# Performance work log

Measured on AMD Instinct MI355X. Metric: run time of the kernel, lower is better.

The kernel has to match this reference:

```python
import jax, jax.numpy as jnp
import numpy as np

LN_EPS = 1e-5


def _conv2d(x, w, b, pad):
    # x: [B,C,H,W], w: [O,I,k,k] (torch OIHW layout)
    out = jax.lax.conv_general_dilated(
        x, w, (1, 1), [(pad, pad), (pad, pad)],
        dimension_numbers=('NCHW', 'OIHW', 'NCHW'))
    return out + b[None, :, None, None]


def _deform_conv2d(x, offset, w, b, k, pad):
    # torchvision.ops.deform_conv2d, offset_groups=1, stride=1, dilation=1.
    # offset layout: [B, 2*k*k, H, W] with (dy, dx) interleaved per kernel tap.
    B, C, H, W = x.shape
    off = offset.reshape(B, k * k, 2, H, W)
    dy, dx = off[:, :, 0], off[:, :, 1]                      # [B,kk,H,W]
    ky, kx = jnp.meshgrid(jnp.arange(k, dtype=x.dtype),
                          jnp.arange(k, dtype=x.dtype), indexing='ij')
    py = (jnp.arange(H, dtype=x.dtype)[None, None, :, None]
          - pad + ky.reshape(-1)[None, :, None, None] + dy)   # sample rows
    px = (jnp.arange(W, dtype=x.dtype)[None, None, None, :]
          - pad + kx.reshape(-1)[None, :, None, None] + dx)   # sample cols
    y0 = jnp.floor(py)
    x0 = jnp.floor(px)
    fy = py - y0
    fx = px - x0
    xf = x.reshape(B, C, H * W)
    gather = jax.vmap(lambda xb, ib: xb[:, ib])               # [C,HW],[K]->[C,K]

    def corner(yc, xc, wt):
        valid = (yc >= 0) & (yc < H) & (xc >= 0) & (xc < W)
        idx = (jnp.clip(yc, 0, H - 1) * W
               + jnp.clip(xc, 0, W - 1)).astype(jnp.int32).reshape(B, -1)
        g = gather(xf, idx).reshape(B, C, k * k, H, W)
        return g * (wt * valid.astype(x.dtype))[:, None]

    # bilinear sample with zero padding outside the image
    acc = (corner(y0, x0, (1 - fy) * (1 - fx))
           + corner(y0, x0 + 1, (1 - fy) * fx)
           + corner(y0 + 1, x0, fy * (1 - fx))
           + corner(y0 + 1, x0 + 1, fy * fx))                 # [B,C,kk,H,W]
    out = jnp.einsum('bckhw,ock->bohw', acc, w.reshape(w.shape[0], C, k * k))
    return out + b[None, :, None, None]


def _deform_branch(xs, off_w, off_b, conv_w, conv_b, k, pad):
    # DeformableConv2d.forward: offset conv, deform_conv2d with conv's own
    # weight/bias, then the plain conv applied AGAIN on the result.
    offset = _conv2d(xs, off_w, off_b, pad)
    d = _deform_conv2d(xs, offset, conv_w, conv_b, k, pad)
    return _conv2d(d, conv_w, conv_b, pad)


def reference(x, H, W, fc1_w, fc1_b, off3_w, off3_b, conv3_w, conv3_b,
              off5_w, off5_b, conv5_w, conv5_b, ln_g, ln_b, fc2_w, fc2_b):
    B, N, _ = x.shape
    h = x @ fc1_w.T + fc1_b                                  # [B,N,hid]
    C = h.shape[-1]
    C2 = C // 2
    x1 = jnp.transpose(h[..., :C2], (0, 2, 1)).reshape(B, C2, H, W)
    x2 = jnp.transpose(h[..., C2:], (0, 2, 1)).reshape(B, C2, H, W)
    x1 = _deform_branch(x1, off3_w, off3_b, conv3_w, conv3_b, 3, 1)
    x2 = _deform_branch(x2, off5_w, off5_b, conv5_w, conv5_b, 5, 2)
    y = jnp.concatenate([x1, x2], axis=1)                    # [B,C,H,W]
    y = jnp.transpose(y.reshape(B, C, N), (0, 2, 1))         # [B,N,C]
    mu = jnp.mean(y, axis=-1, keepdims=True)
    var = jnp.mean(jnp.square(y - mu), axis=-1, keepdims=True)
    y = (y - mu) * jax.lax.rsqrt(var + LN_EPS) * ln_g + ln_b
    y = jax.nn.gelu(y, approximate=False)                    # nn.GELU default
    return y @ fc2_w.T + fc2_b


def setup_inputs() -> dict:
    key = jax.random.key(0)
    ks = jax.random.split(key, 16)
    B, H, W, Cin, Chid = 4, 32, 32, 256, 1024
    C2 = Chid // 2
    N = H * W
    r = lambda k, s, sc: jax.random.normal(k, s, dtype=jnp.float32) * sc
    return {
        'x': r(ks[0], (B, N, Cin), 1.0),
        'H': H, 'W': W,
        'fc1_w': r(ks[1], (Chid, Cin), 0.02),
        'fc1_b': r(ks[2], (Chid,), 0.02),
        'off3_w': r(ks[3], (2 * 9, C2, 3, 3), 0.01),
        'off3_b': r(ks[4], (2 * 9,), 0.01),
        'conv3_w': r(ks[5], (C2, C2, 3, 3), 0.02),
        'conv3_b': r(ks[6], (C2,), 0.02),
        'off5_w': r(ks[7], (2 * 25, C2, 5, 5), 0.01),
        'off5_b': r(ks[8], (2 * 25,), 0.01),
        'conv5_w': r(ks[9], (C2, C2, 5, 5), 0.02),
        'conv5_b': r(ks[10], (C2,), 0.02),
        'ln_g': jnp.ones((Chid,), jnp.float32),
        'ln_b': jnp.zeros((Chid,), jnp.float32),
        'fc2_w': r(ks[11], (Cin, Chid), 0.02),
        'fc2_b': r(ks[12], (Cin,), 0.02),
    }
```

## Files before the change

### kernel.cpp

```cpp
#include <hip/hip_runtime.h>

#define B_    4
#define H_    32
#define W_    32
#define N_    1024
#define CIN_  256
#define CHID_ 1024
#define C2_   512

typedef __attribute__((ext_vector_type(8))) short short8b;
typedef __attribute__((ext_vector_type(4))) float f32x4;

__device__ __forceinline__ unsigned int f2bf2(float lo, float hi) {
    unsigned int ul = __float_as_uint(lo);
    unsigned int uh = __float_as_uint(hi);
    ul += 0x7fffu + ((ul >> 16) & 1u);
    uh += 0x7fffu + ((uh >> 16) & 1u);
    return (ul >> 16) | (uh & 0xffff0000u);
}
__device__ __forceinline__ unsigned short f2bf(float f) {
    unsigned int u = __float_as_uint(f);
    u += 0x7fffu + ((u >> 16) & 1u);
    return (unsigned short)(u >> 16);
}
__device__ __forceinline__ float bflo(unsigned int u) { return __uint_as_float(u << 16); }
__device__ __forceinline__ float bfhi(unsigned int u) { return __uint_as_float(u & 0xffff0000u); }

#define ROWP 40
#define MFMA_(a, b, c) __builtin_amdgcn_mfma_f32_16x16x32_bf16(a, b, c, 0, 0, 0)

template<int X> struct Log2 { static constexpr int v = 1 + Log2<X/2>::v; };
template<> struct Log2<1> { static constexpr int v = 0; };

struct ASet { uint4 r0, r1, r2, r3; float4 cw; };
struct BSet { short8b b0, b1, b2, b3; };

template<int AMODE, int KS, int CH, int OUTMODE, int GX>
__global__ __launch_bounds__(512, 2)
void cgemm(const void* __restrict__ Asrc, int lda,
           const unsigned short* __restrict__ Bp, int nk32,
           int tcnt, int KK,
           const float* __restrict__ bias, void* __restrict__ Cout,
           int ldo, int O, int nO16,
           const short4* __restrict__ cidx, const float4* __restrict__ cwt)
{
    constexpr int CHS = Log2<CH>::v;
    __shared__ unsigned short As[2][2][64 * ROWP];

    const int tid = threadIdx.x;
    int m0, o0, tbeg, zslab;
    if constexpr (GX > 0) {
        const int bid = blockIdx.x;
        o0 = (bid & (GX - 1)) * 128;
        m0 = (bid / GX) * 64;
        tbeg = 0; zslab = 0;
    } else {
        o0 = 0;
        m0 = blockIdx.y * 64;
        zslab = blockIdx.z;
        tbeg = zslab * tcnt;
    }

    const int srow = tid >> 3;
    const int sk8  = (tid & 7) << 3;
    const int am = m0 + srow;
    const int an = am & (N_ - 1), ab = am >> 10;
    const int ay = an >> 5, ax = an & 31;

    const int lane = tid & 63, wid = tid >> 6;
    const int wr = (wid >> 2) * 32, wc = (wid & 3) * 32;
    const int l15 = lane & 15, lk = (lane >> 4) * 8;

    const int o16a = min((o0 + wc) >> 4, nO16 - 1);
    const int o16b = min((o0 + wc + 16) >> 4, nO16 - 1);
    const unsigned short* bbA = Bp + (size_t)o16a * nk32 * 512 + lane * 8;
    const unsigned short* bbB = Bp + (size_t)o16b * nk32 * 512 + lane * 8;

    const int T = tcnt << CHS;
    const int qbase = (tbeg << CHS) * 2;

    const float* fp = nullptr;
    const unsigned short* sp = nullptr;
    bool svalid = false;
    const unsigned short *g0p = nullptr, *g1p = nullptr,
                         *g2p = nullptr, *g3p = nullptr;
    float4 curCw = {0.f, 0.f, 0.f, 0.f};
    short4 ciPref = {0, 0, 0, 0};
    float4 cwPref = {0.f, 0.f, 0.f, 0.f};

    if constexpr (AMODE == 0) {
        fp = (const float*)Asrc + (size_t)am * lda + sk8;
    } else if constexpr (AMODE == 2) {
        ciPref = cidx[(size_t)am * KK + tbeg];
        cwPref = cwt [(size_t)am * KK + tbeg];
    }

    auto advanceTap = [&](int tp) {
        if constexpr (AMODE == 1) {
            const int PAD = KS / 2;
            const int ty = tp / KS, tx = tp - ty * KS;
            const int yy = ay + ty - PAD, xx = ax + tx - PAD;
            svalid = (yy >= 0 && yy < H_ && xx >= 0 && xx < W_);
            if (svalid)
                sp = (const unsigned short*)Asrc
                   + (size_t)((ab << 10) | (yy << 5) | xx) * lda + sk8;
        } else if constexpr (AMODE == 2) {
            const unsigned short* base = (const unsigned short*)Asrc;
            g0p = base + (size_t)(int)ciPref.x * lda + sk8;
            g1p = base + (size_t)(int)ciPref.y * lda + sk8;
            g2p = base + (size_t)(int)ciPref.z * lda + sk8;
            g3p = base + (size_t)(int)ciPref.w * lda + sk8;
            curCw = cwPref;
            ciPref = cidx[(size_t)am * KK + tp + 1];
            cwPref = cwt [(size_t)am * KK + tp + 1];
        }
    };

    auto loadRaw = [&](ASet& S, int u) {
        if constexpr (AMODE == 0) {
            S.r0 = *(const uint4*)(fp + (u << 6));
            S.r1 = *(const uint4*)(fp + (u << 6) + 4);
        } else if constexpr (AMODE == 1) {
            S.r0 = svalid ? *(const uint4*)(sp + (u << 6))
                          : make_uint4(0u, 0u, 0u, 0u);
        } else {
            S.r0 = *(const uint4*)(g0p + (u << 6));
            S.r1 = *(const uint4*)(g1p + (u << 6));
            S.r2 = *(const uint4*)(g2p + (u << 6));
            S.r3 = *(const uint4*)(g3p + (u << 6));
            S.cw = curCw;
        }
    };

    auto bl1 = [](unsigned a, unsigned b, unsigned c, unsigned d, float4 cw) {
        const float lo = cw.x * bflo(a) + cw.y * bflo(b)
                       + cw.z * bflo(c) + cw.w * bflo(d);
        const float hi = cw.x * bfhi(a) + cw.y * bfhi(b)
                       + cw.z * bfhi(c) + cw.w * bfhi(d);
        return f2bf2(lo, hi);
    };

    auto blendWrite = [&](ASet& S, int buf) {
        uint4 o;
        if constexpr (AMODE == 0) {
            o = make_uint4(f2bf2(__uint_as_float(S.r0.x), __uint_as_float(S.r0.y)),
                           f2bf2(__uint_as_float(S.r0.z), __uint_as_float(S.r0.w)),
                           f2bf2(__uint_as_float(S.r1.x), __uint_as_float(S.r1.y)),
                           f2bf2(__uint_as_float(S.r1.z), __uint_as_float(S.r1.w)));
        } else if constexpr (AMODE == 1) {
            o = S.r0;
        } else {
            o = make_uint4(bl1(S.r0.x, S.r1.x, S.r2.x, S.r3.x, S.cw),
                           bl1(S.r0.y, S.r1.y, S.r2.y, S.r3.y, S.cw),
                           bl1(S.r0.z, S.r1.z, S.r2.z, S.r3.z, S.cw),
                           bl1(S.r0.w, S.r1.w, S.r2.w, S.r3.w, S.cw));
        }
        *(uint4*)&As[buf][sk8 >> 5][srow * ROWP + (sk8 & 31)] = o;
    };

    auto loadB = [&](BSet& Bv, int g) {
        const int q = qbase + 2 * g;
        Bv.b0 = *(const short8b*)(bbA + (size_t)q * 512);
        Bv.b1 = *(const short8b*)(bbA + (size_t)(q + 1) * 512);
        Bv.b2 = *(const short8b*)(bbB + (size_t)q * 512);
        Bv.b3 = *(const short8b*)(bbB + (size_t)(q + 1) * 512);
    };

    f32x4 acc[2][2];
#pragma unroll
    for (int i = 0; i < 2; ++i)
#pragma unroll
        for (int j = 0; j < 2; ++j)
            acc[i][j] = (f32x4){0.f, 0.f, 0.f, 0.f};

    ASet S0, S1; BSet B0, B1;

    advanceTap(tbeg);
    {
        ASet P;
        loadRaw(P, 0);
        blendWrite(P, 0);
    }
    loadRaw(S0, 1);
    loadB(B0, 0);
    __syncthreads();

    int cur = 0;

    auto iter = [&](int g, ASet& N, ASet& F, BSet& bc, BSet& bn) {
        if (g + 1 < T) loadB(bn, g + 1);
        if (g + 2 < T) {
            const int gn = g + 2;
            if ((gn & (CH - 1)) == 0) advanceTap(tbeg + (gn >> CHS));
            loadRaw(F, gn & (CH - 1));
        }
        if (g + 1 < T) blendWrite(N, cur ^ 1);

        const unsigned short* a0 = As[cur][0];
        const unsigned short* a1 = As[cur][1];
        const short8b af00 = *(const short8b*)(a0 + (wr      + l15) * ROWP + lk);
        const short8b af01 = *(const short8b*)(a0 + (wr + 16 + l15) * ROWP + lk);
        const short8b af10 = *(const short8b*)(a1 + (wr      + l15) * ROWP + lk);
        const short8b af11 = *(const short8b*)(a1 + (wr + 16 + l15) * ROWP + lk);

        acc[0][0] = MFMA_(af00, bc.b0, acc[0][0]);
        acc[0][1] = MFMA_(af00, bc.b2, acc[0][1]);
        acc[1][0] = MFMA_(af01, bc.b0, acc[1][0]);
        acc[1][1] = MFMA_(af01, bc.b2, acc[1][1]);
        acc[0][0] = MFMA_(af10, bc.b1, acc[0][0]);
        acc[0][1] = MFMA_(af10, bc.b3, acc[0][1]);
        acc[1][0] = MFMA_(af11, bc.b1, acc[1][0]);
        acc[1][1] = MFMA_(af11, bc.b3, acc[1][1]);

        __syncthreads();
        cur ^= 1;
    };

    for (int g = 0; g < T; g += 2) {
        iter(g,     S0, S1, B0, B1);
        iter(g + 1, S1, S0, B1, B0);
    }

    const int row0 = m0 + wr + (lane >> 4) * 4;
    const int col0 = o0 + wc + l15;
#pragma unroll
    for (int j = 0; j < 2; ++j) {
        const int cc = col0 + j * 16;
        if (cc < O) {
#pragma unroll
            for (int i = 0; i < 2; ++i)
#pragma unroll
                for (int r = 0; r < 4; ++r) {
                    const int row = row0 + i * 16 + r;
                    if constexpr (OUTMODE == 0)
                        ((float*)Cout)[(size_t)row * ldo + cc] = acc[i][j][r] + bias[cc];
                    else if constexpr (OUTMODE == 1)
                        ((unsigned short*)Cout)[(size_t)row * ldo + cc] =
                            f2bf(acc[i][j][r] + bias[cc]);
                    else
                        ((float*)Cout)[(size_t)zslab * (B_ * N_) * 64
                                       + (size_t)row * 64 + cc] = acc[i][j][r];
                }
        }
    }
}

__global__ void pack_w(const float* __restrict__ w, unsigned short* __restrict__ dst,
                       int Ovalid, int Opad, int obase, int Kc, int KK, int t0, int Ktot)
{
    const int gid = blockIdx.x * blockDim.x + threadIdx.x;
    if (gid >= Opad * Ktot) return;
    const int k  = gid % Ktot;
    const int od = gid / Ktot;
    float v = 0.f;
    if (od < Ovalid) {
        const size_t o = obase + od;
        if (KK == 1) {
            v = w[o * Kc + k];
        } else {
            const int t = t0 + (k >> 9);
            const int c = k & 511;
            v = w[(o * Kc + c) * KK + t];
        }
    }
    const int o16 = od >> 4, l = od & 15, k32 = k >> 5;
    const size_t di = ((size_t)(o16 * (Ktot >> 5) + k32) * 64
                       + (l + ((k >> 3) & 3) * 16)) * 8 + (k & 7);
    dst[di] = f2bf(v);
}

__global__ void pack_conv(const float* __restrict__ w, unsigned short* __restrict__ dst,
                          int O, int KK)
{
    const int gid = blockIdx.x * blockDim.x + threadIdx.x;
    if (gid >= O * 256) return;
    const int c2 = gid & 255;
    const int o  = gid >> 8;
    const int c  = c2 << 1;
    const float* src = w + ((size_t)o * 512 + c) * KK;
    const int nk32 = KK << 4;
    const int o16 = o >> 4, l = o & 15;
    for (int t = 0; t < KK; ++t) {
        const float v0 = src[t];
        const float v1 = src[KK + t];
        const int k = t * 512 + c;
        const size_t di = ((size_t)(o16 * nk32 + (k >> 5)) * 64
                           + (l + ((k >> 3) & 3) * 16)) * 8 + (k & 7);
        *(unsigned int*)&dst[di] = f2bf2(v0, v1);
    }
}

template<int KS, int Z>
__global__ void coeff_kernel(const float* __restrict__ offp,
                             const float* __restrict__ ob,
                             short4* __restrict__ cidx, float4* __restrict__ cwt)
{
    const int KK = KS * KS, PAD = KS / 2;
    const int gid = blockIdx.x * blockDim.x + threadIdx.x;
    if (gid >= B_ * N_ * KK) return;
    const int t = gid % KK;
    const int n = (gid / KK) & (N_ - 1);
    const int b = gid / (KK * N_);
    const int mtok = b * N_ + n;

    const int SL = B_ * N_ * 64;
    float dy = ob[2 * t], dx = ob[2 * t + 1];
#pragma unroll
    for (int z = 0; z < Z; ++z) {
        dy += offp[(size_t)z * SL + (size_t)mtok * 64 + 2 * t];
        dx += offp[(size_t)z * SL + (size_t)mtok * 64 + 2 * t + 1];
    }

    const int y = n >> 5, x = n & 31;
    const float py = (float)(y - PAD + t / KS) + dy;
    const float px = (float)(x - PAD + t % KS) + dx;
    const float y0f = floorf(py), x0f = floorf(px);
    const float fy = py - y0f, fx = px - x0f;
    const int y0 = (int)y0f, x0 = (int)x0f;

    int idx[4]; float wt[4];
    const int   yy[4] = {y0, y0, y0 + 1, y0 + 1};
    const int   xx[4] = {x0, x0 + 1, x0, x0 + 1};
    const float ww[4] = {(1.f - fy) * (1.f - fx), (1.f - fy) * fx,
                         fy * (1.f - fx),         fy * fx};
#pragma unroll
    for (int r = 0; r < 4; ++r) {
        const bool v = (yy[r] >= 0 && yy[r] < H_ && xx[r] >= 0 && xx[r] < W_);
        const int yc = min(max(yy[r], 0), H_ - 1);
        const int xc = min(max(xx[r], 0), W_ - 1);
        idx[r] = b * N_ + yc * W_ + xc;
        wt[r] = v ? ww[r] : 0.f;
    }
    cidx[(size_t)mtok * KK + t] =
        make_short4((short)idx[0], (short)idx[1], (short)idx[2], (short)idx[3]);
    cwt[(size_t)mtok * KK + t] = make_float4(wt[0], wt[1], wt[2], wt[3]);
}

__global__ __launch_bounds__(256)
void ln_gelu(float* __restrict__ ytok, const float* __restrict__ g,
             const float* __restrict__ bt)
{
    const int t = blockIdx.x;
    const int tid = threadIdx.x;
    float* row = ytok + (size_t)t * CHID_;

    float4 v = *(const float4*)&row[tid << 2];
    __shared__ float red[4];

    float s = v.x + v.y + v.z + v.w;
#pragma unroll
    for (int o = 32; o > 0; o >>= 1) s += __shfl_down(s, o, 64);
    if ((tid & 63) == 0) red[tid >> 6] = s;
    __syncthreads();
    const float mean = (red[0] + red[1] + red[2] + red[3]) * (1.f / CHID_);

    const float d0 = v.x - mean, d1 = v.y - mean, d2 = v.z - mean, d3 = v.w - mean;
    float q = d0 * d0 + d1 * d1 + d2 * d2 + d3 * d3;
#pragma unroll
    for (int o = 32; o > 0; o >>= 1) q += __shfl_down(q, o, 64);
    __syncthreads();
    if ((tid & 63) == 0) red[tid >> 6] = q;
    __syncthreads();
    const float var = (red[0] + red[1] + red[2] + red[3]) * (1.f / CHID_);
    const float rstd = rsqrtf(var + 1e-5f);

    const float4 gv = *(const float4*)&g[tid << 2];
    const float4 bv = *(const float4*)&bt[tid << 2];
    float o0 = d0 * rstd * gv.x + bv.x;
    float o1 = d1 * rstd * gv.y + bv.y;
    float o2 = d2 * rstd * gv.z + bv.z;
    float o3 = d3 * rstd * gv.w + bv.w;
    o0 = 0.5f * o0 * (1.f + erff(o0 * 0.70710678118654752f));
    o1 = 0.5f * o1 * (1.f + erff(o1 * 0.70710678118654752f));
    o2 = 0.5f * o2 * (1.f + erff(o2 * 0.70710678118654752f));
    o3 = 0.5f * o3 * (1.f + erff(o3 * 0.70710678118654752f));
    *(float4*)&row[tid << 2] = make_float4(o0, o1, o2, o3);
}

extern "C" void kernel_launch(void* const* d_in, const int* in_sizes, int n_in,
                              void* d_out, int out_size, void* d_ws, size_t ws_size,
                              hipStream_t stream) {
    const float* x       = (const float*)d_in[0];
    const float* fc1_w   = (const float*)d_in[3];
    const float* fc1_b   = (const float*)d_in[4];
    const float* off3_w  = (const float*)d_in[5];
    const float* off3_b  = (const float*)d_in[6];
    const float* conv3_w = (const float*)d_in[7];
    const float* conv3_b = (const float*)d_in[8];
    const float* off5_w  = (const float*)d_in[9];
    const float* off5_b  = (const float*)d_in[10];
    const float* conv5_w = (const float*)d_in[11];
    const float* conv5_b = (const float*)d_in[12];
    const float* ln_g    = (const float*)d_in[13];
    const float* ln_b    = (const float*)d_in[14];
    const float* fc2_w   = (const float*)d_in[15];
    const float* fc2_b   = (const float*)d_in[16];
    float* out = (float*)d_out;

    char* ws = (char*)d_ws;
    float*          ytok   = (float*)(ws);
    float*          offp   = (float*)(ws);
    short4*         cidx3  = (short4*)(ws + 5242880);
    float4*         cwt3   = (float4*)(ws + 5537792);
    short4*         cidx5  = (short4*)(ws + 16777216);
    float4*         cwt5   = (float4*)(ws + 17596416);
    unsigned short* hb     = (unsigned short*)(ws + 19234816);
    unsigned short* fc1wb  = (unsigned short*)(ws + 27623424);
    unsigned short* off3wb = (unsigned short*)(ws + 28147712);
    unsigned short* off5wb = (unsigned short*)(ws + 28737536);
    unsigned short* daccb  = (unsigned short*)(ws + 27623424);
    unsigned short* fc2wb  = (unsigned short*)(ws + 31817728);
    unsigned short* conv3wb= (unsigned short*)(ws + 32342016);
    unsigned short* conv5wb= (unsigned short*)(ws + 37060608);

    const dim3 TB(256);
    const dim3 TG(512);

    pack_w<<<(1024*256 + 255)/256, TB, 0, stream>>>(fc1_w, fc1wb, 1024, 1024, 0, 256, 1, 0, 256);
    pack_w<<<(256*1024 + 255)/256, TB, 0, stream>>>(fc2_w, fc2wb, 256, 256, 0, 1024, 1, 0, 1024);
    pack_w<<<(64*4608  + 255)/256, TB, 0, stream>>>(off3_w, off3wb, 18, 64, 0, 512, 9, 0, 4608);
    pack_w<<<(64*12800 + 255)/256, TB, 0, stream>>>(off5_w, off5wb, 50, 64, 0, 512, 25, 0, 12800);
    pack_conv<<<(512*256 + 255)/256, TB, 0, stream>>>(conv3_w, conv3wb, 512, 9);
    pack_conv<<<(512*256 + 255)/256, TB, 0, stream>>>(conv5_w, conv5wb, 512, 25);

    cgemm<0,1,4,1,8><<<8*64, TG, 0, stream>>>(
        x, CIN_, fc1wb, 8, 1, 1, fc1_b, hb, CHID_, CHID_, 64, nullptr, nullptr);

    cgemm<1,3,8,2,0><<<dim3(1,64,3), TG, 0, stream>>>(
        hb, CHID_, off3wb, 144, 3, 1, nullptr, offp, 64, 18, 4, nullptr, nullptr);
    coeff_kernel<3,3><<<(B_*N_*9 + 255)/256, TB, 0, stream>>>(offp, off3_b, cidx3, cwt3);
    cgemm<1,5,8,2,0><<<dim3(1,64,5), TG, 0, stream>>>(
        hb + C2_, CHID_, off5wb, 400, 5, 1, nullptr, offp, 64, 50, 4, nullptr, nullptr);
    coeff_kernel<5,5><<<(B_*N_*25 + 255)/256, TB, 0, stream>>>(offp, off5_b, cidx5, cwt5);

    cgemm<2,3,8,1,4><<<4*64, TG, 0, stream>>>(
        hb, CHID_, conv3wb, 144, 9, 9, conv3_b, daccb, C2_, C2_, 32, cidx3, cwt3);
    cgemm<1,3,8,0,4><<<4*64, TG, 0, stream>>>(
        daccb, C2_, conv3wb, 144, 9, 1, conv3_b, ytok, CHID_, C2_, 32, nullptr, nullptr);

    cgemm<2,5,8,1,4><<<4*64, TG, 0, stream>>>(
        hb + C2_, CHID_, conv5wb, 400, 25, 25, conv5_b, daccb, C2_, C2_, 32, cidx5, cwt5);
    cgemm<1,5,8,0,4><<<4*64, TG, 0, stream>>>(
        daccb, C2_, conv5wb, 400, 25, 1, conv5_b, ytok + C2_, CHID_, C2_, 32, nullptr, nullptr);

    ln_gelu<<<B_*N_, TB, 0, stream>>>(ytok, ln_g, ln_b);
    cgemm<0,1,16,0,2><<<2*64, TG, 0, stream>>>(
        ytok, CHID_, fc2wb, 32, 1, 1, fc2_b, out, CIN_, CIN_, 16, nullptr, nullptr);
}
```

Measured before the change: 699.5 us.

## Remap conv GEMM block order for XCD locality, use hardware bf16 pack, guard prefetch

Adds an IMGX block-index remap for the four conv GEMMs so that blocks sharing rows and output tiles land on the same XCD (bid&7) and cover neighbouring 2x2 tile groups, aiming to improve L2 reuse of the A tiles and weights. It replaces the software round-to-nearest bf16 packing with the v_cvt_pk_bf16_f32 instruction in the blend and fp32-convert paths, cutting ALU work. It also stops the coefficient prefetch from reading past the last tap of a slab, which avoids out-of-range loads.

```diff
diff --git a/kernel.cpp b/kernel.cpp
--- a/kernel.cpp
+++ b/kernel.cpp
@@ -23,6 +23,11 @@
     u += 0x7fffu + ((u >> 16) & 1u);
     return (unsigned short)(u >> 16);
 }
+__device__ __forceinline__ unsigned int cvtpk(float lo, float hi) {
+    unsigned int r;
+    asm("v_cvt_pk_bf16_f32 %0, %1, %2" : "=v"(r) : "v"(lo), "v"(hi));
+    return r;
+}
 __device__ __forceinline__ float bflo(unsigned int u) { return __uint_as_float(u << 16); }
 __device__ __forceinline__ float bfhi(unsigned int u) { return __uint_as_float(u & 0xffff0000u); }
 
@@ -35,7 +40,7 @@
 struct ASet { uint4 r0, r1, r2, r3; float4 cw; };
 struct BSet { short8b b0, b1, b2, b3; };
 
-template<int AMODE, int KS, int CH, int OUTMODE, int GX>
+template<int AMODE, int KS, int CH, int OUTMODE, int GX, int IMGX = 0>
 __global__ __launch_bounds__(512, 2)
 void cgemm(const void* __restrict__ Asrc, int lda,
            const unsigned short* __restrict__ Bp, int nk32,
@@ -51,8 +56,14 @@
     int m0, o0, tbeg, zslab;
     if constexpr (GX > 0) {
         const int bid = blockIdx.x;
-        o0 = (bid & (GX - 1)) * 128;
-        m0 = (bid / GX) * 64;
+        if constexpr (IMGX) {
+            const int b8 = bid & 7, rest = bid >> 3;
+            o0 = ((((b8 & 1) << 1) | (rest & 1))) * 128;
+            m0 = (((b8 >> 1) << 4) | (rest >> 1)) * 64;
+        } else {
+            o0 = (bid & (GX - 1)) * 128;
+            m0 = (bid / GX) * 64;
+        }
         tbeg = 0; zslab = 0;
     } else {
         o0 = 0;
@@ -111,8 +122,10 @@
             g2p = base + (size_t)(int)ciPref.z * lda + sk8;
             g3p = base + (size_t)(int)ciPref.w * lda + sk8;
             curCw = cwPref;
-            ciPref = cidx[(size_t)am * KK + tp + 1];
-            cwPref = cwt [(size_t)am * KK + tp + 1];
+            if (tp + 1 < tbeg + tcnt) {
+                ciPref = cidx[(size_t)am * KK + tp + 1];
+                cwPref = cwt [(size_t)am * KK + tp + 1];
+            }
         }
     };
 
@@ -137,16 +150,16 @@
                        + cw.z * bflo(c) + cw.w * bflo(d);
         const float hi = cw.x * bfhi(a) + cw.y * bfhi(b)
                        + cw.z * bfhi(c) + cw.w * bfhi(d);
-        return f2bf2(lo, hi);
+        return cvtpk(lo, hi);
     };
 
     auto blendWrite = [&](ASet& S, int buf) {
         uint4 o;
         if constexpr (AMODE == 0) {
-            o = make_uint4(f2bf2(__uint_as_float(S.r0.x), __uint_as_float(S.r0.y)),
-                           f2bf2(__uint_as_float(S.r0.z), __uint_as_float(S.r0.w)),
-                           f2bf2(__uint_as_float(S.r1.x), __uint_as_float(S.r1.y)),
-                           f2bf2(__uint_as_float(S.r1.z), __uint_as_float(S.r1.w)));
+            o = make_uint4(cvtpk(__uint_as_float(S.r0.x), __uint_as_float(S.r0.y)),
+                           cvtpk(__uint_as_float(S.r0.z), __uint_as_float(S.r0.w)),
+                           cvtpk(__uint_as_float(S.r1.x), __uint_as_float(S.r1.y)),
+                           cvtpk(__uint_as_float(S.r1.z), __uint_as_float(S.r1.w)));
         } else if constexpr (AMODE == 1) {
             o = S.r0;
         } else {
@@ -433,14 +446,14 @@
         hb + C2_, CHID_, off5wb, 400, 5, 1, nullptr, offp, 64, 50, 4, nullptr, nullptr);
     coeff_kernel<5,5><<<(B_*N_*25 + 255)/256, TB, 0, stream>>>(offp, off5_b, cidx5, cwt5);
 
-    cgemm<2,3,8,1,4><<<4*64, TG, 0, stream>>>(
+    cgemm<2,3,8,1,4,1><<<4*64, TG, 0, stream>>>(
         hb, CHID_, conv3wb, 144, 9, 9, conv3_b, daccb, C2_, C2_, 32, cidx3, cwt3);
-    cgemm<1,3,8,0,4><<<4*64, TG, 0, stream>>>(
+    cgemm<1,3,8,0,4,1><<<4*64, TG, 0, stream>>>(
         daccb, C2_, conv3wb, 144, 9, 1, conv3_b, ytok, CHID_, C2_, 32, nullptr, nullptr);
 
-    cgemm<2,5,8,1,4><<<4*64, TG, 0, stream>>>(
+    cgemm<2,5,8,1,4,1><<<4*64, TG, 0, stream>>>(
         hb + C2_, CHID_, conv5wb, 400, 25, 25, conv5_b, daccb, C2_, C2_, 32, cidx5, cwt5);
-    cgemm<1,5,8,0,4><<<4*64, TG, 0, stream>>>(
+    cgemm<1,5,8,0,4,1><<<4*64, TG, 0, stream>>>(
         daccb, C2_, conv5wb, 400, 25, 1, conv5_b, ytok + C2_, CHID_, C2_, 32, nullptr, nullptr);
 
     ln_gelu<<<B_*N_, TB, 0, stream>>>(ytok, ln_g, ln_b);
```

Measured after the change: 676.2 us. 3.3% less time.
